# Performance work log

Hardware: AMD Instinct MI355X
Metric: run time of the kernel (lower is better)

Reference implementation:

```python
import jax, jax.numpy as jnp
import numpy as np

B, C, H, W, N = 32, 256, 56, 56, 1024


def setup_inputs() -> dict:
    key = jax.random.key(0)
    k1, k2, k3, k4 = jax.random.split(key, 4)
    x = jax.random.normal(k1, (B, C, H, W), dtype=jnp.float32)
    W_s = jax.random.normal(k2, (N, H, W), dtype=jnp.float32)
    W_d = jax.random.normal(k3, (N, C, 1, 1), dtype=jnp.float32)
    W_b = jax.random.normal(k4, (1, N), dtype=jnp.float32)
    return {"x": x, "W_s": W_s, "W_d": W_d, "W_b": W_b}


def reference(x, W_s, W_d, W_b):
    # Original: out = einsum('bchw,nhw->bnchw'); per-neuron 1x1 conv with W_d[n]
    # (C -> 1 channel); sum over (c,h,w); add bias. Mathematically:
    #   out[b,n] = sum_{c,h,w} x[b,c,h,w] * W_s[n,h,w] * W_d[n,c] + W_b[0,n]
    # Computed without materializing the (B,N,C,H,W) blow-up:
    y = jnp.einsum('bchw,nhw->bnc', x, W_s)          # spatial contraction
    out = jnp.einsum('bnc,nc->bn', y, W_d[:, :, 0, 0])  # channel contraction
    return out + W_b
```

## Files before the change

kernel.cpp:

```cpp
#include <hip/hip_runtime.h>
#include <stdint.h>


#define K_DIM 3136
#define N_DIM 1024
#define C_DIM 256
#define B_DIM 32
#define M_DIM 8192
#define X_ELEMS (M_DIM * K_DIM)
#define WS_ELEMS (N_DIM * K_DIM)

typedef __attribute__((ext_vector_type(8))) short short8v;
typedef __attribute__((ext_vector_type(4))) float f32x4;

__device__ __forceinline__ short f2bf(float f) {
  union { float f; unsigned u; } v; v.f = f;
  unsigned r = v.u + 0x7FFFu + ((v.u >> 16) & 1u);
  return (short)(r >> 16);
}

__device__ __forceinline__ void async16(const void* g, void* l) {
  __builtin_amdgcn_global_load_lds(
      (const __attribute__((address_space(1))) unsigned int*)g,
      (__attribute__((address_space(3))) unsigned int*)l, 16, 0, 0);
}

#define XBLK (X_ELEMS / 4096)
#define CVBLK ((X_ELEMS + WS_ELEMS) / 4096)
__global__ __launch_bounds__(256) void convert_bf16_bias(
    const float* __restrict__ x, const float* __restrict__ Ws,
    const float* __restrict__ Wb, short* __restrict__ dst,
    float* __restrict__ out) {
  int bid = blockIdx.x;
  if (bid >= CVBLK) {
    int i = (bid - CVBLK) * 256 + threadIdx.x;
    out[i] = Wb[i & (N_DIM - 1)];
    return;
  }
  const float* src;
  short* d;
  size_t base;
  if (bid < XBLK) {
    src = x; d = dst; base = (size_t)bid * 4096;
  } else {
    src = Ws; d = dst + X_ELEMS; base = (size_t)(bid - XBLK) * 4096;
  }
#pragma unroll
  for (int h = 0; h < 2; ++h) {
    size_t i = base + threadIdx.x * 8 + h * 2048;
    f32x4 v0 = __builtin_nontemporal_load((const f32x4*)(src + i));
    f32x4 v1 = __builtin_nontemporal_load((const f32x4*)(src + i) + 1);
    short8v s;
    s[0] = f2bf(v0.x); s[1] = f2bf(v0.y); s[2] = f2bf(v0.z); s[3] = f2bf(v0.w);
    s[4] = f2bf(v1.x); s[5] = f2bf(v1.y); s[6] = f2bf(v1.z); s[7] = f2bf(v1.w);
    *(short8v*)(d + i) = s;
  }
}

__global__ __launch_bounds__(512, 4) void gemm_fused(
    const short* __restrict__ Abf, const short* __restrict__ Bbf,
    const float* __restrict__ Wd, float* __restrict__ out) {
  __shared__ __align__(16) short As[256 * 64];
  __shared__ __align__(16) short Bs[128 * 64];

  const int bid = blockIdx.x;
  const int mt = bid & 31;
  const int nt = (bid >> 5) & 7;
  const int z = bid >> 8;
  const int kt0 = z * 25;
  const int ktn = z ? 24 : 25;

  const int t = threadIdx.x;
  const int lane = t & 63;
  const int wv = t >> 6;
  const int r = lane & 15;
  const int q = lane >> 4;
  const int wm = wv >> 1, wn = wv & 1;

  const int rr = lane >> 3;
  const int k8 = (lane & 7) ^ rr;
  const short* Aw = Abf + (size_t)(mt * 256 + wv * 32 + rr) * K_DIM + k8 * 8 + kt0 * 64;
  const short* Bw = Bbf + (size_t)(nt * 128 + wv * 16 + rr) * K_DIM + k8 * 8 + kt0 * 64;
  char* AsB = (char*)As + wv * 4096;
  char* BsB = (char*)Bs + wv * 2048;

  f32x4 acc[4][4];
#pragma unroll
  for (int i = 0; i < 4; ++i)
#pragma unroll
    for (int j = 0; j < 4; ++j) acc[i][j] = (f32x4)0.0f;

  for (int kt = 0; kt < ktn; ++kt) {
    __syncthreads();
#pragma unroll
    for (int p = 0; p < 4; ++p)
      async16(Aw + (size_t)p * 8 * K_DIM + kt * 64, AsB + p * 1024);
#pragma unroll
    for (int p = 0; p < 2; ++p)
      async16(Bw + (size_t)p * 8 * K_DIM + kt * 64, BsB + p * 1024);
    __syncthreads();

#pragma unroll
    for (int ks = 0; ks < 2; ++ks) {
      const int xo = ((ks * 4 + q) ^ (r & 7)) * 16;
      short8v a[4], b[4];
#pragma unroll
      for (int i = 0; i < 4; ++i)
        a[i] = *(const short8v*)((const char*)As + (64 * wm + 16 * i + r) * 128 + xo);
#pragma unroll
      for (int j = 0; j < 4; ++j)
        b[j] = *(const short8v*)((const char*)Bs + (64 * wn + 16 * j + r) * 128 + xo);
#pragma unroll
      for (int i = 0; i < 4; ++i)
#pragma unroll
        for (int j = 0; j < 4; ++j)
          acc[i][j] = __builtin_amdgcn_mfma_f32_16x16x32_bf16(a[i], b[j],
                                                              acc[i][j], 0, 0, 0);
    }
  }

#pragma unroll
  for (int j = 0; j < 4; ++j) {
    const int n_g = nt * 128 + 64 * wn + 16 * j + r;
    float p = 0.0f;
#pragma unroll
    for (int i = 0; i < 4; ++i) {
      const int c_l = 64 * wm + 16 * i + 4 * q;
      const float4 wd = *(const float4*)(Wd + (size_t)n_g * C_DIM + c_l);
      p += acc[i][j].x * wd.x + acc[i][j].y * wd.y + acc[i][j].z * wd.z +
           acc[i][j].w * wd.w;
    }
    p += __shfl_xor(p, 16, 64);
    p += __shfl_xor(p, 32, 64);
    if (q == 0) atomicAdd(&out[(size_t)mt * N_DIM + n_g], p);
  }
}

extern "C" void kernel_launch(void* const* d_in, const int* in_sizes, int n_in,
                              void* d_out, int out_size, void* d_ws, size_t ws_size,
                              hipStream_t stream) {
  const float* x = (const float*)d_in[0];
  const float* Ws = (const float*)d_in[1];
  const float* Wd = (const float*)d_in[2];
  const float* Wb = (const float*)d_in[3];
  float* out = (float*)d_out;
  short* xbf = (short*)d_ws;

  convert_bf16_bias<<<dim3(CVBLK + 128), dim3(256), 0, stream>>>(x, Ws, Wb, xbf, out);
  gemm_fused<<<dim3(32 * 8 * 2), dim3(512), 0, stream>>>(xbf, xbf + X_ELEMS, Wd, out);
}
```

Baseline: 207.4 us.

## Rewrite GEMM as 256x256 tile with 4-stage async LDS pipeline

The GEMM tile grows from 256x128 to 256x256, and the K step drops to 32 with a 4-deep ring of LDS buffers filled by async global-to-LDS loads issued three tiles ahead. Explicit vmcnt waits, split barriers and s_setprio are used so MFMA work overlaps with loads. The grid halves to 256 blocks at 2 blocks per CU. This targets load latency and the duplicate A reads across N tiles, at the cost of 128KB of LDS, fewer blocks in flight and more accumulator registers.

```diff
diff --git a/kernel.cpp b/kernel.cpp
--- a/kernel.cpp
+++ b/kernel.cpp
@@ -9,6 +9,7 @@
 #define M_DIM 8192
 #define X_ELEMS (M_DIM * K_DIM)
 #define WS_ELEMS (N_DIM * K_DIM)
+#define NSTEP 49
 
 typedef __attribute__((ext_vector_type(8))) short short8v;
 typedef __attribute__((ext_vector_type(4))) float f32x4;
@@ -57,75 +58,108 @@
   }
 }
 
-__global__ __launch_bounds__(512, 4) void gemm_fused(
+
+#define VMCNT(N) asm volatile("s_waitcnt vmcnt(" #N ")" ::: "memory")
+#define CBAR() asm volatile("" ::: "memory")
+#define BARR() { CBAR(); __builtin_amdgcn_s_barrier(); CBAR(); }
+
+#define STAGEA(T) { char* d_ = sm + (((T) & 3) << 15) + (wv << 10);           \
+    const short* g_ = Ag + (size_t)(T) * 32;                                  \
+    async16(g_, d_);                                                          \
+    async16(g_ + (size_t)128 * K_DIM, d_ + 8192); }
+
+#define STAGEB(T) { char* d_ = sm + (((T) & 3) << 15) + 16384 + (wv << 10);   \
+    const short* g_ = Bg + (size_t)(T) * 32;                                  \
+    async16(g_, d_);                                                          \
+    async16(g_ + (size_t)128 * K_DIM, d_ + 8192); }
+
+#define MFQ(F, AV)                                                            \
+  acc[F][0] = __builtin_amdgcn_mfma_f32_16x16x32_bf16(AV, b0, acc[F][0], 0, 0, 0); \
+  acc[F][1] = __builtin_amdgcn_mfma_f32_16x16x32_bf16(AV, b1, acc[F][1], 0, 0, 0); \
+  acc[F][2] = __builtin_amdgcn_mfma_f32_16x16x32_bf16(AV, b2, acc[F][2], 0, 0, 0); \
+  acc[F][3] = __builtin_amdgcn_mfma_f32_16x16x32_bf16(AV, b3, acc[F][3], 0, 0, 0);
+
+#define KTILE(T, STG, VMSTMT)                                                 \
+  {                                                                           \
+    char* sl = sm + (((T) & 3) << 15);                                        \
+    if (STG) STAGEA((T) + 3);                                                 \
+    short8v b0 = *(const short8v*)(sl + boff);                                \
+    short8v b1 = *(const short8v*)(sl + boff + 1024);                         \
+    short8v b2 = *(const short8v*)(sl + boff + 2048);                         \
+    short8v b3 = *(const short8v*)(sl + boff + 3072);                         \
+    short8v a0 = *(const short8v*)(sl + aoff);                                \
+    short8v a1 = *(const short8v*)(sl + aoff + 1024);                         \
+    short8v a2 = *(const short8v*)(sl + aoff + 2048);                         \
+    short8v a3 = *(const short8v*)(sl + aoff + 3072);                         \
+    BARR();                                                                   \
+    __builtin_amdgcn_s_setprio(1);                                            \
+    MFQ(0, a0) MFQ(1, a1) MFQ(2, a2) MFQ(3, a3)                               \
+    __builtin_amdgcn_s_setprio(0);                                            \
+    BARR();                                                                   \
+    if (STG) STAGEB((T) + 3);                                                 \
+    a0 = *(const short8v*)(sl + aoff + 4096);                                 \
+    a1 = *(const short8v*)(sl + aoff + 5120);                                 \
+    a2 = *(const short8v*)(sl + aoff + 6144);                                 \
+    a3 = *(const short8v*)(sl + aoff + 7168);                                 \
+    VMSTMT;                                                                   \
+    __builtin_amdgcn_sched_barrier(0);                                        \
+    BARR();                                                                   \
+    __builtin_amdgcn_s_setprio(1);                                            \
+    MFQ(4, a0) MFQ(5, a1) MFQ(6, a2) MFQ(7, a3)                               \
+    __builtin_amdgcn_s_setprio(0);                                            \
+    BARR();                                                                   \
+  }
+
+__global__ __launch_bounds__(512, 2) void gemm_fused(
     const short* __restrict__ Abf, const short* __restrict__ Bbf,
     const float* __restrict__ Wd, float* __restrict__ out) {
-  __shared__ __align__(16) short As[256 * 64];
-  __shared__ __align__(16) short Bs[128 * 64];
+  __shared__ __align__(16) char sm[131072];
 
   const int bid = blockIdx.x;
   const int mt = bid & 31;
-  const int nt = (bid >> 5) & 7;
-  const int z = bid >> 8;
-  const int kt0 = z * 25;
-  const int ktn = z ? 24 : 25;
+  const int nt = (bid >> 5) & 3;
+  const int z = bid >> 7;
+  const int kt0 = z * NSTEP;
 
-  const int t = threadIdx.x;
-  const int lane = t & 63;
-  const int wv = t >> 6;
+  const int tid = threadIdx.x;
+  const int lane = tid & 63;
+  const int wv = tid >> 6;
   const int r = lane & 15;
   const int q = lane >> 4;
-  const int wm = wv >> 1, wn = wv & 1;
+  const int wm = wv >> 2, wn = wv & 3;
 
-  const int rr = lane >> 3;
-  const int k8 = (lane & 7) ^ rr;
-  const short* Aw = Abf + (size_t)(mt * 256 + wv * 32 + rr) * K_DIM + k8 * 8 + kt0 * 64;
-  const short* Bw = Bbf + (size_t)(nt * 128 + wv * 16 + rr) * K_DIM + k8 * 8 + kt0 * 64;
-  char* AsB = (char*)As + wv * 4096;
-  char* BsB = (char*)Bs + wv * 2048;
+  const int srow = wv * 16 + (lane >> 2);
+  const int sk8 = (lane & 3) ^ ((lane >> 3) & 3);
+  const short* Ag = Abf + (size_t)(mt * 256 + srow) * K_DIM + kt0 * 32 + sk8 * 8;
+  const short* Bg = Bbf + (size_t)(nt * 256 + srow) * K_DIM + kt0 * 32 + sk8 * 8;
 
-  f32x4 acc[4][4];
+  const int swz = (q ^ ((r >> 1) & 3)) << 4;
+  const int aoff = (wm * 128 + r) * 64 + swz;
+  const int boff = 16384 + (wn * 64 + r) * 64 + swz;
+
+  f32x4 acc[8][4];
 #pragma unroll
-  for (int i = 0; i < 4; ++i)
+  for (int i = 0; i < 8; ++i)
 #pragma unroll
     for (int j = 0; j < 4; ++j) acc[i][j] = (f32x4)0.0f;
 
-  for (int kt = 0; kt < ktn; ++kt) {
-    __syncthreads();
-#pragma unroll
-    for (int p = 0; p < 4; ++p)
-      async16(Aw + (size_t)p * 8 * K_DIM + kt * 64, AsB + p * 1024);
-#pragma unroll
-    for (int p = 0; p < 2; ++p)
-      async16(Bw + (size_t)p * 8 * K_DIM + kt * 64, BsB + p * 1024);
-    __syncthreads();
+  STAGEA(0) STAGEB(0) STAGEA(1) STAGEB(1) STAGEA(2) STAGEB(2)
+  VMCNT(8);
+  BARR();
 
-#pragma unroll
-    for (int ks = 0; ks < 2; ++ks) {
-      const int xo = ((ks * 4 + q) ^ (r & 7)) * 16;
-      short8v a[4], b[4];
-#pragma unroll
-      for (int i = 0; i < 4; ++i)
-        a[i] = *(const short8v*)((const char*)As + (64 * wm + 16 * i + r) * 128 + xo);
-#pragma unroll
-      for (int j = 0; j < 4; ++j)
-        b[j] = *(const short8v*)((const char*)Bs + (64 * wn + 16 * j + r) * 128 + xo);
-#pragma unroll
-      for (int i = 0; i < 4; ++i)
-#pragma unroll
-        for (int j = 0; j < 4; ++j)
-          acc[i][j] = __builtin_amdgcn_mfma_f32_16x16x32_bf16(a[i], b[j],
-                                                              acc[i][j], 0, 0, 0);
-    }
-  }
+#pragma unroll 1
+  for (int t = 0; t < NSTEP - 3; ++t) KTILE(t, 1, VMCNT(8));
+  KTILE(NSTEP - 3, 0, VMCNT(4));
+  KTILE(NSTEP - 2, 0, VMCNT(0));
+  KTILE(NSTEP - 1, 0, (void)0);
 
 #pragma unroll
   for (int j = 0; j < 4; ++j) {
-    const int n_g = nt * 128 + 64 * wn + 16 * j + r;
+    const int n_g = nt * 256 + wn * 64 + 16 * j + r;
     float p = 0.0f;
 #pragma unroll
-    for (int i = 0; i < 4; ++i) {
-      const int c_l = 64 * wm + 16 * i + 4 * q;
+    for (int i = 0; i < 8; ++i) {
+      const int c_l = wm * 128 + 16 * i + 4 * q;
       const float4 wd = *(const float4*)(Wd + (size_t)n_g * C_DIM + c_l);
       p += acc[i][j].x * wd.x + acc[i][j].y * wd.y + acc[i][j].z * wd.z +
            acc[i][j].w * wd.w;
@@ -147,5 +181,5 @@
   short* xbf = (short*)d_ws;
 
   convert_bf16_bias<<<dim3(CVBLK + 128), dim3(256), 0, stream>>>(x, Ws, Wb, xbf, out);
-  gemm_fused<<<dim3(32 * 8 * 2), dim3(512), 0, stream>>>(xbf, xbf + X_ELEMS, Wd, out);
+  gemm_fused<<<dim3(32 * 4 * 2), dim3(512), 0, stream>>>(xbf, xbf + X_ELEMS, Wd, out);
 }
```

Result: no change. 209.6 us (+1.1%).

## Pre-pack bf16 operands into MFMA fragment layout and load directly to registers

Applied to the files above, without the earlier changes.

The convert kernel now uses LDS to transpose x and W_s into a fragment-packed layout, so each lane's 16-byte MFMA operand sits contiguously per 16-row by 32-k block. The GEMM then drops LDS and barriers entirely and loads fragments straight from global memory into registers, double-buffered across k-steps. Each block computes a 256x256 tile with 8x4 accumulators per wave over a 256-block grid mapped to XCDs, with MFMA priority raised. This removes LDS staging and syncs but adds redundant global reads of B across waves and higher register pressure.

```diff
diff --git a/kernel.cpp b/kernel.cpp
--- a/kernel.cpp
+++ b/kernel.cpp
@@ -5,10 +5,13 @@
 #define K_DIM 3136
 #define N_DIM 1024
 #define C_DIM 256
-#define B_DIM 32
 #define M_DIM 8192
 #define X_ELEMS (M_DIM * K_DIM)
 #define WS_ELEMS (N_DIM * K_DIM)
+#define OUT_ELEMS (M_DIM / C_DIM * N_DIM)
+#define NKT 98
+#define NSTEP 49
+#define FSTR ((size_t)NKT * 512)
 
 typedef __attribute__((ext_vector_type(8))) short short8v;
 typedef __attribute__((ext_vector_type(4))) float f32x4;
@@ -19,113 +22,153 @@
   return (short)(r >> 16);
 }
 
-__device__ __forceinline__ void async16(const void* g, void* l) {
-  __builtin_amdgcn_global_load_lds(
-      (const __attribute__((address_space(1))) unsigned int*)g,
-      (__attribute__((address_space(3))) unsigned int*)l, 16, 0, 0);
-}
+__global__ __launch_bounds__(256) void convert_pack(
+    const float* __restrict__ x, const float* __restrict__ Ws,
+    const float* __restrict__ Wb, short* __restrict__ Apk,
+    short* __restrict__ Bpk, float* __restrict__ out) {
+  const int ktp = blockIdx.x;
+  const int yg = blockIdx.y;
+  const int t = threadIdx.x;
 
-#define XBLK (X_ELEMS / 4096)
-#define CVBLK ((X_ELEMS + WS_ELEMS) / 4096)
-__global__ __launch_bounds__(256) void convert_bf16_bias(
-    const float* __restrict__ x, const float* __restrict__ Ws,
-    const float* __restrict__ Wb, short* __restrict__ dst,
-    float* __restrict__ out) {
-  int bid = blockIdx.x;
-  if (bid >= CVBLK) {
-    int i = (bid - CVBLK) * 256 + threadIdx.x;
-    out[i] = Wb[i & (N_DIM - 1)];
+  if (yg == 144) {
+    for (int i = ktp * 256 + t; i < OUT_ELEMS; i += 49 * 256)
+      out[i] = Wb[i & (N_DIM - 1)];
     return;
   }
+
+  __shared__ short lds[64][72];
   const float* src;
-  short* d;
-  size_t base;
-  if (bid < XBLK) {
-    src = x; d = dst; base = (size_t)bid * 4096;
-  } else {
-    src = Ws; d = dst + X_ELEMS; base = (size_t)(bid - XBLK) * 4096;
-  }
+  short* dst;
+  int rowbase;
+  if (yg < 128) { src = x;  dst = Apk; rowbase = yg * 64; }
+  else          { src = Ws; dst = Bpk; rowbase = (yg - 128) * 64; }
+
+  const int rr = t >> 2;
+  const int cc = (t & 3) * 16;
+  const float* in = src + (size_t)(rowbase + rr) * K_DIM + ktp * 64 + cc;
+  f32x4 v0 = __builtin_nontemporal_load((const f32x4*)in);
+  f32x4 v1 = __builtin_nontemporal_load((const f32x4*)in + 1);
+  f32x4 v2 = __builtin_nontemporal_load((const f32x4*)in + 2);
+  f32x4 v3 = __builtin_nontemporal_load((const f32x4*)in + 3);
+  short8v s0, s1;
+  s0[0] = f2bf(v0.x); s0[1] = f2bf(v0.y); s0[2] = f2bf(v0.z); s0[3] = f2bf(v0.w);
+  s0[4] = f2bf(v1.x); s0[5] = f2bf(v1.y); s0[6] = f2bf(v1.z); s0[7] = f2bf(v1.w);
+  s1[0] = f2bf(v2.x); s1[1] = f2bf(v2.y); s1[2] = f2bf(v2.z); s1[3] = f2bf(v2.w);
+  s1[4] = f2bf(v3.x); s1[5] = f2bf(v3.y); s1[6] = f2bf(v3.z); s1[7] = f2bf(v3.w);
+  *(short8v*)&lds[rr][cc] = s0;
+  *(short8v*)&lds[rr][cc + 8] = s1;
+  __syncthreads();
+
+  const int f = t >> 5, sub = t & 31;
+  const int rbl = f >> 1, ktl = f & 1;
+  const size_t fb =
+      ((size_t)((rowbase >> 4) + rbl) * NKT + (ktp * 2 + ktl)) * 512;
 #pragma unroll
-  for (int h = 0; h < 2; ++h) {
-    size_t i = base + threadIdx.x * 8 + h * 2048;
-    f32x4 v0 = __builtin_nontemporal_load((const f32x4*)(src + i));
-    f32x4 v1 = __builtin_nontemporal_load((const f32x4*)(src + i) + 1);
-    short8v s;
-    s[0] = f2bf(v0.x); s[1] = f2bf(v0.y); s[2] = f2bf(v0.z); s[3] = f2bf(v0.w);
-    s[4] = f2bf(v1.x); s[5] = f2bf(v1.y); s[6] = f2bf(v1.z); s[7] = f2bf(v1.w);
-    *(short8v*)(d + i) = s;
+  for (int s = 0; s < 2; ++s) {
+    const int l = sub + 32 * s;
+    short8v w = *(const short8v*)&lds[rbl * 16 + (l & 15)][ktl * 32 + (l >> 4) * 8];
+    *(short8v*)(dst + fb + l * 8) = w;
   }
 }
 
-__global__ __launch_bounds__(512, 4) void gemm_fused(
-    const short* __restrict__ Abf, const short* __restrict__ Bbf,
+#define SB0() __builtin_amdgcn_sched_barrier(0)
+
+#define NTL(P) __builtin_nontemporal_load((const short8v*)(P))
+
+#define LOADF(KT) {                                                           \
+    const short* ap_ = Ab + (size_t)(KT) * 512;                               \
+    fa0 = NTL(ap_);            fa1 = NTL(ap_ + FSTR);                         \
+    fa2 = NTL(ap_ + 2 * FSTR); fa3 = NTL(ap_ + 3 * FSTR);                     \
+    fa4 = NTL(ap_ + 4 * FSTR); fa5 = NTL(ap_ + 5 * FSTR);                     \
+    fa6 = NTL(ap_ + 6 * FSTR); fa7 = NTL(ap_ + 7 * FSTR);                     \
+    const short* bp_ = Bb + (size_t)(KT) * 512;                               \
+    fb0 = *(const short8v*)bp_;            fb1 = *(const short8v*)(bp_ + FSTR); \
+    fb2 = *(const short8v*)(bp_ + 2 * FSTR); fb3 = *(const short8v*)(bp_ + 3 * FSTR); \
+    SB0(); }
+
+#define LOADG(KT) {                                                           \
+    const short* ap_ = Ab + (size_t)(KT) * 512;                               \
+    ga0 = NTL(ap_);            ga1 = NTL(ap_ + FSTR);                         \
+    ga2 = NTL(ap_ + 2 * FSTR); ga3 = NTL(ap_ + 3 * FSTR);                     \
+    ga4 = NTL(ap_ + 4 * FSTR); ga5 = NTL(ap_ + 5 * FSTR);                     \
+    ga6 = NTL(ap_ + 6 * FSTR); ga7 = NTL(ap_ + 7 * FSTR);                     \
+    const short* bp_ = Bb + (size_t)(KT) * 512;                               \
+    gb0 = *(const short8v*)bp_;            gb1 = *(const short8v*)(bp_ + FSTR); \
+    gb2 = *(const short8v*)(bp_ + 2 * FSTR); gb3 = *(const short8v*)(bp_ + 3 * FSTR); \
+    SB0(); }
+
+#define M16(A, B, C) __builtin_amdgcn_mfma_f32_16x16x32_bf16(A, B, C, 0, 0, 0)
+
+#define MFROW(J, BV, A0, A1, A2, A3, A4, A5, A6, A7)                          \
+  acc[0][J] = M16(A0, BV, acc[0][J]); acc[1][J] = M16(A1, BV, acc[1][J]);     \
+  acc[2][J] = M16(A2, BV, acc[2][J]); acc[3][J] = M16(A3, BV, acc[3][J]);     \
+  acc[4][J] = M16(A4, BV, acc[4][J]); acc[5][J] = M16(A5, BV, acc[5][J]);     \
+  acc[6][J] = M16(A6, BV, acc[6][J]); acc[7][J] = M16(A7, BV, acc[7][J]);
+
+#define MFMAF                                                                 \
+  __builtin_amdgcn_s_setprio(1);                                              \
+  MFROW(0, fb0, fa0, fa1, fa2, fa3, fa4, fa5, fa6, fa7)                       \
+  MFROW(1, fb1, fa0, fa1, fa2, fa3, fa4, fa5, fa6, fa7)                       \
+  MFROW(2, fb2, fa0, fa1, fa2, fa3, fa4, fa5, fa6, fa7)                       \
+  MFROW(3, fb3, fa0, fa1, fa2, fa3, fa4, fa5, fa6, fa7)                       \
+  __builtin_amdgcn_s_setprio(0);
+
+#define MFMAG                                                                 \
+  __builtin_amdgcn_s_setprio(1);                                              \
+  MFROW(0, gb0, ga0, ga1, ga2, ga3, ga4, ga5, ga6, ga7)                       \
+  MFROW(1, gb1, ga0, ga1, ga2, ga3, ga4, ga5, ga6, ga7)                       \
+  MFROW(2, gb2, ga0, ga1, ga2, ga3, ga4, ga5, ga6, ga7)                       \
+  MFROW(3, gb3, ga0, ga1, ga2, ga3, ga4, ga5, ga6, ga7)                       \
+  __builtin_amdgcn_s_setprio(0);
+
+__global__ __launch_bounds__(512, 2) void gemm_pk(
+    const short* __restrict__ Apk, const short* __restrict__ Bpk,
     const float* __restrict__ Wd, float* __restrict__ out) {
-  __shared__ __align__(16) short As[256 * 64];
-  __shared__ __align__(16) short Bs[128 * 64];
+  const int bid = blockIdx.x;
+  const int xcd = bid & 7;
+  const int nt = xcd >> 1;
+  const int z = xcd & 1;
+  const int mt = bid >> 3;
+  const int ktg0 = z * NSTEP;
 
-  const int bid = blockIdx.x;
-  const int mt = bid & 31;
-  const int nt = (bid >> 5) & 7;
-  const int z = bid >> 8;
-  const int kt0 = z * 25;
-  const int ktn = z ? 24 : 25;
-
-  const int t = threadIdx.x;
-  const int lane = t & 63;
-  const int wv = t >> 6;
+  const int tid = threadIdx.x;
+  const int lane = tid & 63;
+  const int wv = tid >> 6;
   const int r = lane & 15;
   const int q = lane >> 4;
-  const int wm = wv >> 1, wn = wv & 1;
+  const int wm = wv >> 2, wn = wv & 3;
 
-  const int rr = lane >> 3;
-  const int k8 = (lane & 7) ^ rr;
-  const short* Aw = Abf + (size_t)(mt * 256 + wv * 32 + rr) * K_DIM + k8 * 8 + kt0 * 64;
-  const short* Bw = Bbf + (size_t)(nt * 128 + wv * 16 + rr) * K_DIM + k8 * 8 + kt0 * 64;
-  char* AsB = (char*)As + wv * 4096;
-  char* BsB = (char*)Bs + wv * 2048;
+  const short* Ab =
+      Apk + ((size_t)(mt * 16 + wm * 8) * NKT + ktg0) * 512 + lane * 8;
+  const short* Bb =
+      Bpk + ((size_t)(nt * 16 + wn * 4) * NKT + ktg0) * 512 + lane * 8;
 
-  f32x4 acc[4][4];
+  f32x4 acc[8][4];
 #pragma unroll
-  for (int i = 0; i < 4; ++i)
+  for (int i = 0; i < 8; ++i)
 #pragma unroll
     for (int j = 0; j < 4; ++j) acc[i][j] = (f32x4)0.0f;
 
-  for (int kt = 0; kt < ktn; ++kt) {
-    __syncthreads();
-#pragma unroll
-    for (int p = 0; p < 4; ++p)
-      async16(Aw + (size_t)p * 8 * K_DIM + kt * 64, AsB + p * 1024);
-#pragma unroll
-    for (int p = 0; p < 2; ++p)
-      async16(Bw + (size_t)p * 8 * K_DIM + kt * 64, BsB + p * 1024);
-    __syncthreads();
+  short8v fa0, fa1, fa2, fa3, fa4, fa5, fa6, fa7, fb0, fb1, fb2, fb3;
+  short8v ga0, ga1, ga2, ga3, ga4, ga5, ga6, ga7, gb0, gb1, gb2, gb3;
 
-#pragma unroll
-    for (int ks = 0; ks < 2; ++ks) {
-      const int xo = ((ks * 4 + q) ^ (r & 7)) * 16;
-      short8v a[4], b[4];
-#pragma unroll
-      for (int i = 0; i < 4; ++i)
-        a[i] = *(const short8v*)((const char*)As + (64 * wm + 16 * i + r) * 128 + xo);
-#pragma unroll
-      for (int j = 0; j < 4; ++j)
-        b[j] = *(const short8v*)((const char*)Bs + (64 * wn + 16 * j + r) * 128 + xo);
-#pragma unroll
-      for (int i = 0; i < 4; ++i)
-#pragma unroll
-        for (int j = 0; j < 4; ++j)
-          acc[i][j] = __builtin_amdgcn_mfma_f32_16x16x32_bf16(a[i], b[j],
-                                                              acc[i][j], 0, 0, 0);
-    }
+  LOADF(0);
+#pragma unroll 1
+  for (int u = 0; u < 24; ++u) {
+    LOADG(2 * u + 1);
+    MFMAF;
+    LOADF(2 * u + 2);
+    MFMAG;
   }
+  MFMAF;
 
 #pragma unroll
   for (int j = 0; j < 4; ++j) {
-    const int n_g = nt * 128 + 64 * wn + 16 * j + r;
+    const int n_g = nt * 256 + wn * 64 + 16 * j + r;
     float p = 0.0f;
 #pragma unroll
-    for (int i = 0; i < 4; ++i) {
-      const int c_l = 64 * wm + 16 * i + 4 * q;
+    for (int i = 0; i < 8; ++i) {
+      const int c_l = wm * 128 + 16 * i + 4 * q;
       const float4 wd = *(const float4*)(Wd + (size_t)n_g * C_DIM + c_l);
       p += acc[i][j].x * wd.x + acc[i][j].y * wd.y + acc[i][j].z * wd.z +
            acc[i][j].w * wd.w;
@@ -144,8 +187,9 @@
   const float* Wd = (const float*)d_in[2];
   const float* Wb = (const float*)d_in[3];
   float* out = (float*)d_out;
-  short* xbf = (short*)d_ws;
+  short* apk = (short*)d_ws;
+  short* bpk = apk + X_ELEMS;
 
-  convert_bf16_bias<<<dim3(CVBLK + 128), dim3(256), 0, stream>>>(x, Ws, Wb, xbf, out);
-  gemm_fused<<<dim3(32 * 8 * 2), dim3(512), 0, stream>>>(xbf, xbf + X_ELEMS, Wd, out);
+  convert_pack<<<dim3(49, 145), dim3(256), 0, stream>>>(x, Ws, Wb, apk, bpk, out);
+  gemm_pk<<<dim3(256), dim3(512), 0, stream>>>(apk, bpk, Wd, out);
 }
```

New measurement: 278.5 us. 34.3% more time.
